# Optimization experiments

Measured on AMD Instinct MI355X. Metric: run time of the kernel, lower is better.

Reference implementation:

```python
import jax, jax.numpy as jnp
import numpy as np

BATCH_SIZE = 512
NUM_ID = 64
FEAT_DIMS = 512
GROUP = BATCH_SIZE // NUM_ID


def setup_inputs() -> dict:
    key = jax.random.key(0)
    k1, k2 = jax.random.split(key)
    f_s = jax.random.normal(k1, (BATCH_SIZE, FEAT_DIMS), dtype=jnp.float32)
    f_t = jax.random.normal(k2, (BATCH_SIZE, FEAT_DIMS), dtype=jnp.float32)
    return {"f_s": f_s, "f_t": f_t}


def reference(f_s, f_t):
    B, g, n_id = BATCH_SIZE, GROUP, NUM_ID
    # all-pairs similarity: (B, B)
    sim_all = f_s @ f_t.T
    # sim_diff[i, j, k] = sim_all[i, k] - sim_all[i, j]  -> (B, B, B)
    sim_diff = sim_all[:, None, :] - sim_all[:, :, None]
    mask = 1.0 - jnp.eye(B, dtype=sim_all.dtype)  # over (j, k)
    sim_sg = jax.nn.relu(sim_diff) * mask[None, :, :]
    sim_all_rk = jnp.sum(sim_sg, axis=-1) + 1.0  # (B, B)

    # per-class positive similarities
    xs = f_s.reshape(n_id, g, FEAT_DIMS)
    xt = f_t.reshape(n_id, g, FEAT_DIMS)
    sim_pos = jnp.einsum('nid,njd->nij', xs, xt)  # (n_id, g, g)
    # sim_pos_diff[n, i, j, k] = sim_pos[n, i, k] - sim_pos[n, i, j]
    sim_pos_diff = sim_pos[:, :, None, :] - sim_pos[:, :, :, None]
    pos_mask = 1.0 - jnp.eye(g, dtype=sim_pos.dtype)  # over (j, k)
    sim_pos_sg = jax.nn.relu(sim_pos_diff) * pos_mask[None, None, :, :]
    sim_pos_rk = jnp.sum(sim_pos_sg, axis=-1) + 1.0  # (n_id, g, g)

    # block-diagonal (per-id) slices of sim_all_rk: (n_id, g, g)
    blocks = sim_all_rk.reshape(n_id, g, n_id, g)
    idx = jnp.arange(n_id)
    diag_blocks = blocks[idx, :, idx, :]  # (n_id, g, g)

    ap = jnp.sum(sim_pos_rk / diag_blocks) / g / B
    return 1.0 - ap
```

## Files before the change

kernel.cpp:

```cpp
#include <hip/hip_runtime.h>

#define NB 512
#define FD 512
#define GRP 8
#define KSPLIT 4
#define KCH (FD / KSPLIT)
#define KSUB 64
#define TM 64
#define TN 64

__global__ __launch_bounds__(256)
void k_gemm(const float* __restrict__ fs, const float* __restrict__ ft,
            float* __restrict__ simsl, float* __restrict__ out1)
{
    __shared__ float4 Asv[TM * (KSUB / 4)];
    __shared__ float4 Bsv[TN * (KSUB / 4)];

    const int tid  = threadIdx.x;
    const int bid  = blockIdx.x;
    const int ks   = bid >> 6;
    const int tile = bid & 63;
    const int tr   = (tile >> 3) * TM;
    const int tc   = (tile & 7) * TN;
    const int ty   = tid >> 4;
    const int tx   = tid & 15;

    if (bid == 0 && tid == 0) out1[0] = 1.0f;

    float acc[4][4];
    #pragma unroll
    for (int i = 0; i < 4; ++i)
        #pragma unroll
        for (int j = 0; j < 4; ++j) acc[i][j] = 0.f;

    const int k0 = ks * KCH;
    int srow[4], sslot[4];
    #pragma unroll
    for (int u = 0; u < 4; ++u) {
        const int idx = tid + 256 * u;
        srow[u]  = idx >> 4;
        sslot[u] = idx & 15;
    }

    float4 abuf[4], bbuf[4];
    #pragma unroll
    for (int u = 0; u < 4; ++u) {
        abuf[u] = *(const float4*)(fs + (size_t)(tr + srow[u]) * FD + k0 + 4 * sslot[u]);
        bbuf[u] = *(const float4*)(ft + (size_t)(tc + srow[u]) * FD + k0 + 4 * sslot[u]);
    }

    for (int kc = 0; kc < KCH; kc += KSUB) {
        #pragma unroll
        for (int u = 0; u < 4; ++u) {
            const int slot = sslot[u] ^ (srow[u] >> 2);
            Asv[srow[u] * 16 + slot] = abuf[u];
            Bsv[srow[u] * 16 + slot] = bbuf[u];
        }
        __syncthreads();

        if (kc + KSUB < KCH) {
            const int kk = k0 + kc + KSUB;
            #pragma unroll
            for (int u = 0; u < 4; ++u) {
                abuf[u] = *(const float4*)(fs + (size_t)(tr + srow[u]) * FD + kk + 4 * sslot[u]);
                bbuf[u] = *(const float4*)(ft + (size_t)(tc + srow[u]) * FD + kk + 4 * sslot[u]);
            }
        }

        #pragma unroll
        for (int s = 0; s < KSUB / 4; ++s) {
            float4 a[4], b[4];
            #pragma unroll
            for (int i = 0; i < 4; ++i)
                a[i] = Asv[(4 * ty + i) * 16 + (s ^ ty)];
            #pragma unroll
            for (int j = 0; j < 4; ++j)
                b[j] = Bsv[(4 * tx + j) * 16 + (s ^ tx)];
            #pragma unroll
            for (int i = 0; i < 4; ++i)
                #pragma unroll
                for (int j = 0; j < 4; ++j) {
                    acc[i][j] = fmaf(a[i].x, b[j].x, acc[i][j]);
                    acc[i][j] = fmaf(a[i].y, b[j].y, acc[i][j]);
                    acc[i][j] = fmaf(a[i].z, b[j].z, acc[i][j]);
                    acc[i][j] = fmaf(a[i].w, b[j].w, acc[i][j]);
                }
        }
        __syncthreads();
    }

    float* dst = simsl + (size_t)ks * NB * NB;
    #pragma unroll
    for (int i = 0; i < 4; ++i) {
        float4 v = make_float4(acc[i][0], acc[i][1], acc[i][2], acc[i][3]);
        *(float4*)(dst + (size_t)(tr + 4 * ty + i) * NB + tc + 4 * tx) = v;
    }
}

__global__ __launch_bounds__(64)
void k_rank(const float* __restrict__ simsl, float* __restrict__ out1)
{
    const int b = blockIdx.x;
    const int l = threadIdx.x;
    const int n = b >> 3;

    float r[8];
    #pragma unroll
    for (int q = 0; q < 8; ++q) r[q] = 0.f;
    #pragma unroll
    for (int ks = 0; ks < KSPLIT; ++ks) {
        const float* p = simsl + (size_t)ks * NB * NB + (size_t)b * NB + 8 * l;
        float4 u = *(const float4*)(p);
        float4 v = *(const float4*)(p + 4);
        r[0] += u.x; r[1] += u.y; r[2] += u.z; r[3] += u.w;
        r[4] += v.x; r[5] += v.y; r[6] += v.z; r[7] += v.w;
    }

    float s[8];
    #pragma unroll
    for (int q = 0; q < 8; ++q) s[q] = __shfl(r[q], n);

    float a[8];
    #pragma unroll
    for (int q = 0; q < 8; ++q) a[q] = 0.f;
    #pragma unroll
    for (int q = 0; q < 8; ++q)
        #pragma unroll
        for (int jj = 0; jj < 8; ++jj)
            a[q] += fmaxf(r[jj] - s[q], 0.f);

    #pragma unroll
    for (int off = 1; off < 64; off <<= 1)
        #pragma unroll
        for (int q = 0; q < 8; ++q)
            a[q] += __shfl_xor(a[q], off);

    float contrib = 0.f;
    if (l < 8) {
        float rp = 1.f;
        #pragma unroll
        for (int k = 0; k < 8; ++k) rp += fmaxf(s[k] - s[l], 0.f);
        contrib = rp / (1.f + a[l]);
    }
    contrib += __shfl_xor(contrib, 1);
    contrib += __shfl_xor(contrib, 2);
    contrib += __shfl_xor(contrib, 4);
    if (l == 0) atomicAdd(out1, -contrib * (1.f / (GRP * NB)));
}

extern "C" void kernel_launch(void* const* d_in, const int* in_sizes, int n_in,
                              void* d_out, int out_size, void* d_ws, size_t ws_size,
                              hipStream_t stream)
{
    const float* fs = (const float*)d_in[0];
    const float* ft = (const float*)d_in[1];
    float* out   = (float*)d_out;
    float* simsl = (float*)d_ws;

    k_gemm<<<dim3(256), dim3(256), 0, stream>>>(fs, ft, simsl, out);
    k_rank<<<dim3(512), dim3(64), 0, stream>>>(simsl, out);
}
```

Baseline: 76.22 us.

## Replace FP32 SIMT GEMM with split-bf16 MFMA GEMM and block-reduced rank kernel

Inputs are split in a new pre-pass into bf16 hi and lo planes. The similarity matrix is then computed with bf16 MFMA instructions using three products (hh, hl, lh) to approximate fp32 accuracy, replacing the K-split FP32 FMA GEMM. The rank kernel now reads a single sim slice instead of summing four partial slices, and does one atomic per block through shared memory instead of one per wavefront. This adds a third kernel launch and extra plane traffic, and the bf16x3 scheme may lose some precision in the ranking comparisons.

```diff
diff --git a/kernel.cpp b/kernel.cpp
--- a/kernel.cpp
+++ b/kernel.cpp
@@ -1,120 +1,122 @@
 #include <hip/hip_runtime.h>
+
+typedef __attribute__((ext_vector_type(8))) short bf16x8;
+typedef __attribute__((ext_vector_type(4))) float f32x4;
 
 #define NB 512
 #define FD 512
-#define GRP 8
-#define KSPLIT 4
-#define KCH (FD / KSPLIT)
-#define KSUB 64
-#define TM 64
-#define TN 64
+#define PLANE (NB * FD)
+
+__device__ __forceinline__ ushort f2bf(float x) {
+    uint u = __builtin_bit_cast(uint, x);
+    return (ushort)((u + 0x7FFFu + ((u >> 16) & 1u)) >> 16);
+}
+__device__ __forceinline__ float bf2f(ushort h) {
+    uint u = ((uint)h) << 16;
+    return __builtin_bit_cast(float, u);
+}
 
 __global__ __launch_bounds__(256)
-void k_gemm(const float* __restrict__ fs, const float* __restrict__ ft,
-            float* __restrict__ simsl, float* __restrict__ out1)
+void k_split(const float* __restrict__ fs, const float* __restrict__ ft,
+             ushort* __restrict__ planes, float* __restrict__ out1)
 {
-    __shared__ float4 Asv[TM * (KSUB / 4)];
-    __shared__ float4 Bsv[TN * (KSUB / 4)];
+    const int t = blockIdx.x * 256 + threadIdx.x;
+    if (t == 0) out1[0] = 1.0f;
+    const int mat = t >> 16;
+    const int i4  = t & 65535;
+    const float4 v = ((const float4*)(mat ? ft : fs))[i4];
 
-    const int tid  = threadIdx.x;
-    const int bid  = blockIdx.x;
-    const int ks   = bid >> 6;
-    const int tile = bid & 63;
-    const int tr   = (tile >> 3) * TM;
-    const int tc   = (tile & 7) * TN;
-    const int ty   = tid >> 4;
-    const int tx   = tid & 15;
+    ushort4 hi, lo;
+    hi.x = f2bf(v.x); lo.x = f2bf(v.x - bf2f(hi.x));
+    hi.y = f2bf(v.y); lo.y = f2bf(v.y - bf2f(hi.y));
+    hi.z = f2bf(v.z); lo.z = f2bf(v.z - bf2f(hi.z));
+    hi.w = f2bf(v.w); lo.w = f2bf(v.w - bf2f(hi.w));
 
-    if (bid == 0 && tid == 0) out1[0] = 1.0f;
-
-    float acc[4][4];
-    #pragma unroll
-    for (int i = 0; i < 4; ++i)
-        #pragma unroll
-        for (int j = 0; j < 4; ++j) acc[i][j] = 0.f;
-
-    const int k0 = ks * KCH;
-    int srow[4], sslot[4];
-    #pragma unroll
-    for (int u = 0; u < 4; ++u) {
-        const int idx = tid + 256 * u;
-        srow[u]  = idx >> 4;
-        sslot[u] = idx & 15;
-    }
-
-    float4 abuf[4], bbuf[4];
-    #pragma unroll
-    for (int u = 0; u < 4; ++u) {
-        abuf[u] = *(const float4*)(fs + (size_t)(tr + srow[u]) * FD + k0 + 4 * sslot[u]);
-        bbuf[u] = *(const float4*)(ft + (size_t)(tc + srow[u]) * FD + k0 + 4 * sslot[u]);
-    }
-
-    for (int kc = 0; kc < KCH; kc += KSUB) {
-        #pragma unroll
-        for (int u = 0; u < 4; ++u) {
-            const int slot = sslot[u] ^ (srow[u] >> 2);
-            Asv[srow[u] * 16 + slot] = abuf[u];
-            Bsv[srow[u] * 16 + slot] = bbuf[u];
-        }
-        __syncthreads();
-
-        if (kc + KSUB < KCH) {
-            const int kk = k0 + kc + KSUB;
-            #pragma unroll
-            for (int u = 0; u < 4; ++u) {
-                abuf[u] = *(const float4*)(fs + (size_t)(tr + srow[u]) * FD + kk + 4 * sslot[u]);
-                bbuf[u] = *(const float4*)(ft + (size_t)(tc + srow[u]) * FD + kk + 4 * sslot[u]);
-            }
-        }
-
-        #pragma unroll
-        for (int s = 0; s < KSUB / 4; ++s) {
-            float4 a[4], b[4];
-            #pragma unroll
-            for (int i = 0; i < 4; ++i)
-                a[i] = Asv[(4 * ty + i) * 16 + (s ^ ty)];
-            #pragma unroll
-            for (int j = 0; j < 4; ++j)
-                b[j] = Bsv[(4 * tx + j) * 16 + (s ^ tx)];
-            #pragma unroll
-            for (int i = 0; i < 4; ++i)
-                #pragma unroll
-                for (int j = 0; j < 4; ++j) {
-                    acc[i][j] = fmaf(a[i].x, b[j].x, acc[i][j]);
-                    acc[i][j] = fmaf(a[i].y, b[j].y, acc[i][j]);
-                    acc[i][j] = fmaf(a[i].z, b[j].z, acc[i][j]);
-                    acc[i][j] = fmaf(a[i].w, b[j].w, acc[i][j]);
-                }
-        }
-        __syncthreads();
-    }
-
-    float* dst = simsl + (size_t)ks * NB * NB;
-    #pragma unroll
-    for (int i = 0; i < 4; ++i) {
-        float4 v = make_float4(acc[i][0], acc[i][1], acc[i][2], acc[i][3]);
-        *(float4*)(dst + (size_t)(tr + 4 * ty + i) * NB + tc + 4 * tx) = v;
-    }
+    ushort4* hp = (ushort4*)(planes + (size_t)mat * 2 * PLANE);
+    ushort4* lp = (ushort4*)(planes + (size_t)mat * 2 * PLANE + PLANE);
+    hp[i4] = hi;
+    lp[i4] = lo;
 }
 
 __global__ __launch_bounds__(64)
-void k_rank(const float* __restrict__ simsl, float* __restrict__ out1)
+void k_mm(const ushort* __restrict__ planes, float* __restrict__ sim)
 {
-    const int b = blockIdx.x;
-    const int l = threadIdx.x;
-    const int n = b >> 3;
+    const int l   = threadIdx.x;
+    const int bid = blockIdx.x;
+    const int tr  = (bid >> 4) * 32;
+    const int tc  = (bid & 15) * 32;
+    const int r0  = l & 15;
+    const int kg  = (l >> 4) * 8;
 
-    float r[8];
+    const ushort* fsh = planes;
+    const ushort* fsl = planes + PLANE;
+    const ushort* fth = planes + 2 * PLANE;
+    const ushort* ftl = planes + 3 * PLANE;
+
+    const ushort* pa0h = fsh + (size_t)(tr + r0)      * FD + kg;
+    const ushort* pa1h = fsh + (size_t)(tr + r0 + 16) * FD + kg;
+    const ushort* pa0l = fsl + (size_t)(tr + r0)      * FD + kg;
+    const ushort* pa1l = fsl + (size_t)(tr + r0 + 16) * FD + kg;
+    const ushort* pb0h = fth + (size_t)(tc + r0)      * FD + kg;
+    const ushort* pb1h = fth + (size_t)(tc + r0 + 16) * FD + kg;
+    const ushort* pb0l = ftl + (size_t)(tc + r0)      * FD + kg;
+    const ushort* pb1l = ftl + (size_t)(tc + r0 + 16) * FD + kg;
+
+    f32x4 acc[2][2];
     #pragma unroll
-    for (int q = 0; q < 8; ++q) r[q] = 0.f;
+    for (int i = 0; i < 2; ++i)
+        #pragma unroll
+        for (int j = 0; j < 2; ++j) acc[i][j] = (f32x4){0.f, 0.f, 0.f, 0.f};
+
+    #pragma unroll 4
+    for (int k = 0; k < FD; k += 32) {
+        const bf16x8 a0h = *(const bf16x8*)(pa0h + k);
+        const bf16x8 a1h = *(const bf16x8*)(pa1h + k);
+        const bf16x8 a0l = *(const bf16x8*)(pa0l + k);
+        const bf16x8 a1l = *(const bf16x8*)(pa1l + k);
+        const bf16x8 b0h = *(const bf16x8*)(pb0h + k);
+        const bf16x8 b1h = *(const bf16x8*)(pb1h + k);
+        const bf16x8 b0l = *(const bf16x8*)(pb0l + k);
+        const bf16x8 b1l = *(const bf16x8*)(pb1l + k);
+
+        acc[0][0] = __builtin_amdgcn_mfma_f32_16x16x32_bf16(a0h, b0h, acc[0][0], 0, 0, 0);
+        acc[0][0] = __builtin_amdgcn_mfma_f32_16x16x32_bf16(a0h, b0l, acc[0][0], 0, 0, 0);
+        acc[0][0] = __builtin_amdgcn_mfma_f32_16x16x32_bf16(a0l, b0h, acc[0][0], 0, 0, 0);
+        acc[0][1] = __builtin_amdgcn_mfma_f32_16x16x32_bf16(a0h, b1h, acc[0][1], 0, 0, 0);
+        acc[0][1] = __builtin_amdgcn_mfma_f32_16x16x32_bf16(a0h, b1l, acc[0][1], 0, 0, 0);
+        acc[0][1] = __builtin_amdgcn_mfma_f32_16x16x32_bf16(a0l, b1h, acc[0][1], 0, 0, 0);
+        acc[1][0] = __builtin_amdgcn_mfma_f32_16x16x32_bf16(a1h, b0h, acc[1][0], 0, 0, 0);
+        acc[1][0] = __builtin_amdgcn_mfma_f32_16x16x32_bf16(a1h, b0l, acc[1][0], 0, 0, 0);
+        acc[1][0] = __builtin_amdgcn_mfma_f32_16x16x32_bf16(a1l, b0h, acc[1][0], 0, 0, 0);
+        acc[1][1] = __builtin_amdgcn_mfma_f32_16x16x32_bf16(a1h, b1h, acc[1][1], 0, 0, 0);
+        acc[1][1] = __builtin_amdgcn_mfma_f32_16x16x32_bf16(a1h, b1l, acc[1][1], 0, 0, 0);
+        acc[1][1] = __builtin_amdgcn_mfma_f32_16x16x32_bf16(a1l, b1h, acc[1][1], 0, 0, 0);
+    }
+
+    const int rbase = (l >> 4) * 4;
     #pragma unroll
-    for (int ks = 0; ks < KSPLIT; ++ks) {
-        const float* p = simsl + (size_t)ks * NB * NB + (size_t)b * NB + 8 * l;
-        float4 u = *(const float4*)(p);
-        float4 v = *(const float4*)(p + 4);
-        r[0] += u.x; r[1] += u.y; r[2] += u.z; r[3] += u.w;
-        r[4] += v.x; r[5] += v.y; r[6] += v.z; r[7] += v.w;
-    }
+    for (int mh = 0; mh < 2; ++mh)
+        #pragma unroll
+        for (int j = 0; j < 4; ++j) {
+            const int row = tr + mh * 16 + rbase + j;
+            sim[(size_t)row * NB + tc + r0]      = acc[mh][0][j];
+            sim[(size_t)row * NB + tc + 16 + r0] = acc[mh][1][j];
+        }
+}
+
+__global__ __launch_bounds__(512)
+void k_rank(const float* __restrict__ sim, float* __restrict__ out1)
+{
+    __shared__ float part[8];
+    const int w = threadIdx.x >> 6;
+    const int l = threadIdx.x & 63;
+    const int n = blockIdx.x;
+    const int b = n * 8 + w;
+
+    const float* p = sim + (size_t)b * NB + 8 * l;
+    const float4 u = *(const float4*)(p);
+    const float4 v = *(const float4*)(p + 4);
+    float r[8] = {u.x, u.y, u.z, u.w, v.x, v.y, v.z, v.w};
 
     float s[8];
     #pragma unroll
@@ -145,7 +147,15 @@
     contrib += __shfl_xor(contrib, 1);
     contrib += __shfl_xor(contrib, 2);
     contrib += __shfl_xor(contrib, 4);
-    if (l == 0) atomicAdd(out1, -contrib * (1.f / (GRP * NB)));
+    if (l == 0) part[w] = contrib;
+    __syncthreads();
+
+    if (threadIdx.x == 0) {
+        float t = 0.f;
+        #pragma unroll
+        for (int i = 0; i < 8; ++i) t += part[i];
+        atomicAdd(out1, -t * (1.f / (8.f * NB)));
+    }
 }
 
 extern "C" void kernel_launch(void* const* d_in, const int* in_sizes, int n_in,
@@ -154,9 +164,12 @@
 {
     const float* fs = (const float*)d_in[0];
     const float* ft = (const float*)d_in[1];
-    float* out   = (float*)d_out;
-    float* simsl = (float*)d_ws;
+    float* out = (float*)d_out;
 
-    k_gemm<<<dim3(256), dim3(256), 0, stream>>>(fs, ft, simsl, out);
-    k_rank<<<dim3(512), dim3(64), 0, stream>>>(simsl, out);
+    ushort* planes = (ushort*)d_ws;
+    float*  sim    = (float*)((char*)d_ws + 4ull * PLANE * sizeof(ushort));
+
+    k_split<<<dim3(512), dim3(256), 0, stream>>>(fs, ft, planes, out);
+    k_mm   <<<dim3(256), dim3(64),  0, stream>>>(planes, sim);
+    k_rank <<<dim3(64),  dim3(512), 0, stream>>>(sim, out);
 }
```

After: 70.24 us. 7.9% less time.
